# Kernel tuning notes

Hardware: AMD Instinct MI355X
Metric: run time of the kernel (lower is better)

Reference implementation:

```python
import jax, jax.numpy as jnp
import numpy as np

DIM = 768
HEADS = 12
HIDDEN = 3072  # dim * mlp_ratio
EPS = 1e-5


def layernorm(x, g, b):
    mu = jnp.mean(x, axis=-1, keepdims=True)
    var = jnp.var(x, axis=-1, keepdims=True)
    return (x - mu) * jax.lax.rsqrt(var + EPS) * g + b


def setup_inputs() -> dict:
    key = jax.random.key(0)
    ks = jax.random.split(key, 10)
    s = 0.02
    return {
        "x": jax.random.normal(ks[0], (4, 1024, DIM), jnp.float32),
        "attention_mask": jax.random.randint(ks[1], (4, 1024), 0, 2, jnp.int32),
        "ln1_g": jnp.ones((DIM,), jnp.float32),
        "ln1_b": jnp.zeros((DIM,), jnp.float32),
        "ln2_g": jnp.ones((DIM,), jnp.float32),
        "ln2_b": jnp.zeros((DIM,), jnp.float32),
        "w_qkv": jax.random.normal(ks[2], (DIM, 3 * DIM), jnp.float32) * s,
        "b_qkv": jnp.zeros((3 * DIM,), jnp.float32),
        "w_proj": jax.random.normal(ks[3], (DIM, DIM), jnp.float32) * s,
        "b_proj": jnp.zeros((DIM,), jnp.float32),
        "w_fc1": jax.random.normal(ks[4], (DIM, HIDDEN), jnp.float32) * s,
        "b_fc1": jnp.zeros((HIDDEN,), jnp.float32),
        "w_fc2": jax.random.normal(ks[5], (HIDDEN, DIM), jnp.float32) * s,
        "b_fc2": jnp.zeros((DIM,), jnp.float32),
    }


def reference(x, attention_mask, ln1_g, ln1_b, ln2_g, ln2_b,
              w_qkv, b_qkv, w_proj, b_proj, w_fc1, b_fc1, w_fc2, b_fc2):
    B, N, C = x.shape
    hd = C // HEADS
    scale = hd ** -0.5

    # --- attention branch ---
    h = layernorm(x, ln1_g, ln1_b)
    qkv = (h @ w_qkv + b_qkv).reshape(B, N, 3, HEADS, hd)
    q, k, v = qkv[:, :, 0], qkv[:, :, 1], qkv[:, :, 2]  # [B,N,H,hd]
    attn = jnp.einsum('bnhd,bmhd->bhnm', q, k) * scale
    mask_bias = jnp.where(attention_mask == 0, -10000.0, 0.0)[:, None, None, :]
    attn = jax.nn.softmax(attn + mask_bias, axis=-1)
    o = jnp.einsum('bhnm,bmhd->bnhd', attn, v).reshape(B, N, C)
    x = x + (o @ w_proj + b_proj)

    # --- MLP branch ---
    h = layernorm(x, ln2_g, ln2_b)
    h = jax.nn.gelu(h @ w_fc1 + b_fc1, approximate=False)
    x = x + (h @ w_fc2 + b_fc2)
    return x
```

## Files before the change

### kernel.cpp

```cpp
#include <hip/hip_runtime.h>

#define DIM 768
#define NTOK 4096
#define HID 3072

typedef __attribute__((ext_vector_type(8))) short bf16x8;
typedef __attribute__((ext_vector_type(4))) float f32x4;

__device__ inline unsigned short f2bf(float f){
  unsigned u = __float_as_uint(f);
  u += 0x7fff + ((u >> 16) & 1);
  return (unsigned short)(u >> 16);
}
__device__ inline unsigned cvt_pk_bf16(float a, float b){
  unsigned r;
  asm("v_cvt_pk_bf16_f32 %0, %1, %2" : "=v"(r) : "v"(a), "v"(b));
  return r;
}
__device__ inline void gload_lds16(const void* g, void* l){
  __builtin_amdgcn_global_load_lds(
      (const __attribute__((address_space(1))) unsigned int*)g,
      (__attribute__((address_space(3))) unsigned int*)l, 16, 0, 0);
}
template<int N> __device__ inline void wait_vmcnt(){
  if constexpr (N == 0) asm volatile("s_waitcnt vmcnt(0)" ::: "memory");
  else if constexpr (N == 4) asm volatile("s_waitcnt vmcnt(4)" ::: "memory");
  else if constexpr (N == 8) asm volatile("s_waitcnt vmcnt(8)" ::: "memory");
  else static_assert(N == 0, "unsupported vmcnt");
}

__global__ __launch_bounds__(256) void ln_kernel(const float* __restrict__ x,
    const float* __restrict__ g, const float* __restrict__ b,
    unsigned short* __restrict__ out)
{
  int row = blockIdx.x * 4 + (threadIdx.x >> 6);
  int lane = threadIdx.x & 63;
  const float* xr = x + (size_t)row * DIM;
  float4 v[3];
  float s = 0.f, s2 = 0.f;
#pragma unroll
  for (int j = 0; j < 3; ++j){
    v[j] = *(const float4*)(xr + j * 256 + lane * 4);
    s  += v[j].x + v[j].y + v[j].z + v[j].w;
    s2 += v[j].x*v[j].x + v[j].y*v[j].y + v[j].z*v[j].z + v[j].w*v[j].w;
  }
#pragma unroll
  for (int m = 1; m < 64; m <<= 1){ s += __shfl_xor(s, m, 64); s2 += __shfl_xor(s2, m, 64); }
  float mu  = s * (1.f / 768.f);
  float var = s2 * (1.f / 768.f) - mu * mu;
  float inv = rsqrtf(var + 1e-5f);
#pragma unroll
  for (int j = 0; j < 3; ++j){
    int c0 = j * 256 + lane * 4;
    float vv[4] = { v[j].x, v[j].y, v[j].z, v[j].w };
    ushort4 o4;
    o4.x = f2bf((vv[0] - mu) * inv * g[c0 + 0] + b[c0 + 0]);
    o4.y = f2bf((vv[1] - mu) * inv * g[c0 + 1] + b[c0 + 1]);
    o4.z = f2bf((vv[2] - mu) * inv * g[c0 + 2] + b[c0 + 2]);
    o4.w = f2bf((vv[3] - mu) * inv * g[c0 + 3] + b[c0 + 3]);
    *(ushort4*)(out + (size_t)row * DIM + c0) = o4;
  }
}

__global__ __launch_bounds__(256) void transpose4_kernel(
    const float* __restrict__ w_qkv, const float* __restrict__ w_proj,
    const float* __restrict__ w_fc1, const float* __restrict__ w_fc2,
    unsigned short* __restrict__ tq, unsigned short* __restrict__ tp,
    unsigned short* __restrict__ t1, unsigned short* __restrict__ t2)
{
  __shared__ __align__(16) unsigned short tile[32][33];
  int id = blockIdx.x;
  const float* W; unsigned short* Wt; int K, N, tx_n;
  if (id < 1728)      { W = w_qkv;  Wt = tq; K = 768;  N = 2304; tx_n = 72; }
  else if (id < 2304) { W = w_proj; Wt = tp; K = 768;  N = 768;  tx_n = 24; id -= 1728; }
  else if (id < 4608) { W = w_fc1;  Wt = t1; K = 768;  N = 3072; tx_n = 96; id -= 2304; }
  else                { W = w_fc2;  Wt = t2; K = 3072; N = 768;  tx_n = 24; id -= 4608; }
  int n0 = (id % tx_n) * 32, k0 = (id / tx_n) * 32;
  int tx = threadIdx.x & 31, ty = threadIdx.x >> 5;
#pragma unroll
  for (int i = 0; i < 32; i += 8)
    tile[ty + i][tx] = f2bf(W[(size_t)(k0 + ty + i) * N + n0 + tx]);
  __syncthreads();
#pragma unroll
  for (int i = 0; i < 32; i += 8)
    Wt[(size_t)(n0 + ty + i) * K + k0 + tx] = tile[tx][ty + i];
}

__global__ __launch_bounds__(256) void pack_mask_kernel(const int* __restrict__ am,
    unsigned long long* __restrict__ pm)
{
  int lane = threadIdx.x & 63, w = threadIdx.x >> 6, b = blockIdx.x;
  for (int k = w; k < 16; k += 4){
    unsigned long long m = __ballot(am[b * 1024 + k * 64 + lane] != 0);
    if (lane == 0) pm[b * 16 + k] = m;
  }
}

template<int DEPTH, int EPI, typename OutT>
__global__ __launch_bounds__(256) void gemm_kernel(
    const unsigned short* __restrict__ A,
    const unsigned short* __restrict__ Bt,
    const float* __restrict__ bias,
    const float* __restrict__ resid,
    OutT* __restrict__ C,
    unsigned short* __restrict__ q_out,
    unsigned short* __restrict__ k_out,
    unsigned short* __restrict__ v_out,
    int M, int N, int K)
{
  constexpr int BM = 128, BN = 128, BK = 32, WM = 64, WN = 64;
  constexpr int WAVES_N = BN / WN;
  constexpr int MI = WM / 16, NI = WN / 16;
  constexpr int ACH = BM * BK / 8, BCH = BN * BK / 8;
  constexpr int NC = (ACH + BCH) / 256;
  constexpr int SMEM_B = DEPTH * (BM + BN) * BK * 2;
  __shared__ __align__(16) char smem[SMEM_B];
  auto As = (unsigned short(*)[BM * BK])smem;
  auto Bs = (unsigned short(*)[BN * BK])(smem + DEPTH * BM * BK * 2);
  const int t = threadIdx.x, lane = t & 63, wid = t >> 6;
  const int lo = lane & 15, hi = lane >> 4;
  const int wr = wid / WAVES_N, wc = wid % WAVES_N;

  const int gx = gridDim.x;
  const int nwg = gx * gridDim.y;
  const int lin = blockIdx.y * gx + blockIdx.x;
  const int swz = (lin & 7) * (nwg >> 3) + (lin >> 3);
  const int bm = (swz / gx) * BM, bn = (swz % gx) * BN;

  auto stage = [&](int buf, int k0){
#pragma unroll
    for (int u = 0; u < NC; ++u){
      int c = u * 256 + t;
      if (c < ACH){
        gload_lds16(A + (size_t)(bm + (c >> 2)) * K + k0 + (c & 3) * 8, &As[buf][c * 8]);
      } else {
        int c2 = c - ACH;
        gload_lds16(Bt + (size_t)(bn + (c2 >> 2)) * K + k0 + (c2 & 3) * 8, &Bs[buf][c2 * 8]);
      }
    }
  };

  f32x4 acc[MI][NI];
#pragma unroll
  for (int i = 0; i < MI; ++i)
#pragma unroll
    for (int j = 0; j < NI; ++j) acc[i][j] = (f32x4){0.f, 0.f, 0.f, 0.f};

  const int NIT = K / BK;
#pragma unroll
  for (int d = 0; d < DEPTH - 1; ++d) stage(d, d * BK);
  for (int it = 0; it < NIT; ++it){
    int rem = NIT - 1 - it;
    if (rem >= DEPTH - 2) wait_vmcnt<(DEPTH - 2) * NC>();
    else if (DEPTH == 4 && rem == 1) wait_vmcnt<NC>();
    else wait_vmcnt<0>();
    __builtin_amdgcn_sched_barrier(0);
    __builtin_amdgcn_s_barrier();
    __builtin_amdgcn_sched_barrier(0);
    if (it + DEPTH - 1 < NIT) stage((it + DEPTH - 1) % DEPTH, (it + DEPTH - 1) * BK);
    const unsigned short* as = As[it % DEPTH];
    const unsigned short* bs = Bs[it % DEPTH];
    bf16x8 af[MI], bfr[NI];
#pragma unroll
    for (int i = 0; i < MI; ++i)  af[i]  = *(const bf16x8*)&as[(wr * WM + i * 16 + lo) * BK + hi * 8];
#pragma unroll
    for (int j = 0; j < NI; ++j) bfr[j] = *(const bf16x8*)&bs[(wc * WN + j * 16 + lo) * BK + hi * 8];
#pragma unroll
    for (int i = 0; i < MI; ++i)
#pragma unroll
      for (int j = 0; j < NI; ++j)
        acc[i][j] = __builtin_amdgcn_mfma_f32_16x16x32_bf16(af[i], bfr[j], acc[i][j], 0, 0, 0);
  }

  __syncthreads();

  if constexpr (EPI == 2){
    constexpr int LDE = BN + 4;
    float* ET = (float*)smem;
#pragma unroll
    for (int half = 0; half < 2; ++half){
      if (wr == half){
#pragma unroll
        for (int i = 0; i < MI; ++i)
#pragma unroll
          for (int j = 0; j < NI; ++j){
            float bcol = bias[bn + wc * WN + j * 16 + lo];
#pragma unroll
            for (int r = 0; r < 4; ++r)
              ET[(i * 16 + hi * 4 + r) * LDE + wc * WN + j * 16 + lo] = acc[i][j][r] + bcol;
          }
      }
      __syncthreads();
      int lrow = t >> 2, gg = t & 3;
      const float* rrow = resid + (size_t)(bm + half * 64 + lrow) * N + bn;
      float* crow = (float*)C + (size_t)(bm + half * 64 + lrow) * N + bn;
#pragma unroll
      for (int k = 0; k < 8; ++k){
        int c4 = (gg + k * 4) * 4;
        float4 v = *(const float4*)&ET[lrow * LDE + c4];
        float4 rs = *(const float4*)&rrow[c4];
        v.x += rs.x; v.y += rs.y; v.z += rs.z; v.w += rs.w;
        *(float4*)&crow[c4] = v;
      }
      if (half == 0) __syncthreads();
    }
  } else if constexpr (EPI == 0 || EPI == 1){
    constexpr int LDE = BN + 8;
    unsigned short* ET = (unsigned short*)smem;
#pragma unroll
    for (int i = 0; i < MI; ++i)
#pragma unroll
      for (int j = 0; j < NI; ++j){
        float bcol = bias[bn + wc * WN + j * 16 + lo];
#pragma unroll
        for (int r = 0; r < 4; ++r){
          float v = acc[i][j][r] + bcol;
          if constexpr (EPI == 1) v = 0.5f * v * (1.f + erff(v * 0.70710678118f));
          ET[(wr * WM + i * 16 + hi * 4 + r) * LDE + wc * WN + j * 16 + lo] = f2bf(v);
        }
      }
    __syncthreads();
#pragma unroll
    for (int p = 0; p < BM / 16; ++p){
      int row = p * 16 + (t >> 4), chunk = t & 15;
      *(bf16x8*)&((unsigned short*)C)[(size_t)(bm + row) * N + bn + chunk * 8] =
          *(const bf16x8*)&ET[row * LDE + chunk * 8];
    }
  } else {
    constexpr int LDE = BN + 8;
    unsigned short* ET = (unsigned short*)smem;
    const int part = bn / 768;
    const int cloc = bn % 768;
#pragma unroll
    for (int i = 0; i < MI; ++i)
#pragma unroll
      for (int j = 0; j < NI; ++j){
        int col_l = wc * WN + j * 16 + lo;
        float bcol = bias[bn + col_l];
#pragma unroll
        for (int r = 0; r < 4; ++r){
          int row_l = wr * WM + i * 16 + hi * 4 + r;
          unsigned short us = f2bf(acc[i][j][r] + bcol);
          if (part < 2) ET[row_l * LDE + col_l] = us;
          else          ET[col_l * LDE + row_l] = us;
        }
      }
    __syncthreads();
    const int bb = bm >> 10, n0b = bm & 1023;
    if (part < 2){
      unsigned short* dst0 = (part == 0) ? q_out : k_out;
#pragma unroll
      for (int p = 0; p < 8; ++p){
        int row = p * 16 + (t >> 4), chunk = t & 15;
        int hh = cloc / 64 + (chunk >> 3), d0 = (chunk & 7) * 8;
        unsigned short* dst = dst0 + ((size_t)(bb * 12 + hh)) * 65536 + (n0b + row) * 64 + d0;
        *(bf16x8*)dst = *(const bf16x8*)&ET[row * LDE + chunk * 8];
      }
    } else {
#pragma unroll
      for (int p = 0; p < 8; ++p){
        int colg = p * 16 + (t >> 4), chunk = t & 15;
        int hh = cloc / 64 + (colg >> 6), d = colg & 63;
        unsigned short* dst = v_out + ((size_t)(bb * 12 + hh)) * 65536 + (size_t)d * 1024 + n0b + chunk * 8;
        *(bf16x8*)dst = *(const bf16x8*)&ET[colg * LDE + chunk * 8];
      }
    }
  }
}

__global__ __launch_bounds__(256) void attn_kernel(
    const unsigned short* __restrict__ Qs,
    const unsigned short* __restrict__ Ks,
    const unsigned short* __restrict__ Vts,
    const unsigned long long* __restrict__ pm,
    unsigned short* __restrict__ o)
{
  constexpr int LD = 72;
  __shared__ __align__(16) unsigned short Kl[64 * LD];
  __shared__ __align__(16) unsigned short Vt[64 * LD];
  __shared__ __align__(16) unsigned short Pl[4][16 * LD];
  const int qb = blockIdx.x, h = blockIdx.y, b = blockIdx.z;
  const int t = threadIdx.x, wid = t >> 6, lane = t & 63;
  const int lo = lane & 15, hi = lane >> 4;
  const size_t bh = (size_t)b * 12 + h;

  const unsigned short* Qg = Qs + (bh * 1024 + qb * 64 + wid * 16 + lo) * 64;
  bf16x8 qf0 = *(const bf16x8*)(Qg + hi * 8);
  bf16x8 qf1 = *(const bf16x8*)(Qg + 32 + hi * 8);

  f32x4 oacc[4];
#pragma unroll
  for (int dj = 0; dj < 4; ++dj) oacc[dj] = (f32x4){0.f, 0.f, 0.f, 0.f};
  float l_part = 0.f;

  const int srow = t >> 2, scol = (t & 3) * 16;
  const unsigned short* Kg = Ks  + bh * 65536;
  const unsigned short* Vg = Vts + bh * 65536;
  unsigned short* pw = &Pl[wid][0];

  for (int kt = 0; kt < 16; ++kt){
    __syncthreads();
    const unsigned short* kg = Kg + (kt * 64 + srow) * 64 + scol;
    *(bf16x8*)&Kl[srow * LD + scol]     = *(const bf16x8*)kg;
    *(bf16x8*)&Kl[srow * LD + scol + 8] = *(const bf16x8*)(kg + 8);
    const unsigned short* vg = Vg + srow * 1024 + kt * 64 + scol;
    *(bf16x8*)&Vt[srow * LD + scol]     = *(const bf16x8*)vg;
    *(bf16x8*)&Vt[srow * LD + scol + 8] = *(const bf16x8*)(vg + 8);
    __syncthreads();

    f32x4 s[4];
#pragma unroll
    for (int nj = 0; nj < 4; ++nj) s[nj] = (f32x4){0.f, 0.f, 0.f, 0.f};
#pragma unroll
    for (int kk = 0; kk < 2; ++kk){
      bf16x8 q = kk ? qf1 : qf0;
#pragma unroll
      for (int nj = 0; nj < 4; ++nj){
        bf16x8 kf = *(const bf16x8*)&Kl[(nj * 16 + lo) * LD + kk * 32 + hi * 8];
        s[nj] = __builtin_amdgcn_mfma_f32_16x16x32_bf16(kf, q, s[nj], 0, 0, 0);
      }
    }

    unsigned long long w = pm[b * 16 + kt] >> (hi * 4);
#pragma unroll
    for (int nj = 0; nj < 4; ++nj){
      float p[4];
#pragma unroll
      for (int r = 0; r < 4; ++r){
        float e = __expf(fmaf(s[nj][r], 0.125f, -16.0f));
        e = ((unsigned)(w >> (nj * 16 + r)) & 1u) ? e : 0.0f;
        l_part += e;
        p[r] = e;
      }
      unsigned w0 = cvt_pk_bf16(p[0], p[1]);
      unsigned w1 = cvt_pk_bf16(p[2], p[3]);
      *(uint2*)&pw[lo * LD + nj * 16 + hi * 4] = make_uint2(w0, w1);
    }
    asm volatile("" ::: "memory");
    bf16x8 pf0 = *(const bf16x8*)&pw[lo * LD + hi * 8];
    bf16x8 pf1 = *(const bf16x8*)&pw[lo * LD + 32 + hi * 8];
#pragma unroll
    for (int kk = 0; kk < 2; ++kk){
      bf16x8 pf = kk ? pf1 : pf0;
#pragma unroll
      for (int dj = 0; dj < 4; ++dj){
        bf16x8 vf = *(const bf16x8*)&Vt[(dj * 16 + lo) * LD + kk * 32 + hi * 8];
        oacc[dj] = __builtin_amdgcn_mfma_f32_16x16x32_bf16(vf, pf, oacc[dj], 0, 0, 0);
      }
    }
  }

  float l = l_part;
  l += __shfl_xor(l, 16, 64);
  l += __shfl_xor(l, 32, 64);
  float inv = 1.0f / l;
  size_t orow = (size_t)b * 1024 + qb * 64 + wid * 16 + lo;
#pragma unroll
  for (int dj = 0; dj < 4; ++dj){
    unsigned w0 = (unsigned)f2bf(oacc[dj][0] * inv) | ((unsigned)f2bf(oacc[dj][1] * inv) << 16);
    unsigned w1 = (unsigned)f2bf(oacc[dj][2] * inv) | ((unsigned)f2bf(oacc[dj][3] * inv) << 16);
    *(uint2*)&o[orow * DIM + h * 64 + dj * 16 + hi * 4] = make_uint2(w0, w1);
  }
}

extern "C" void kernel_launch(void* const* d_in, const int* in_sizes, int n_in,
                              void* d_out, int out_size, void* d_ws, size_t ws_size,
                              hipStream_t stream)
{
  const float* x      = (const float*)d_in[0];
  const int*   amask  = (const int*)  d_in[1];
  const float* ln1_g  = (const float*)d_in[2];
  const float* ln1_b  = (const float*)d_in[3];
  const float* ln2_g  = (const float*)d_in[4];
  const float* ln2_b  = (const float*)d_in[5];
  const float* w_qkv  = (const float*)d_in[6];
  const float* b_qkv  = (const float*)d_in[7];
  const float* w_proj = (const float*)d_in[8];
  const float* b_proj = (const float*)d_in[9];
  const float* w_fc1  = (const float*)d_in[10];
  const float* b_fc1  = (const float*)d_in[11];
  const float* w_fc2  = (const float*)d_in[12];
  const float* b_fc2  = (const float*)d_in[13];
  float* outp = (float*)d_out;

  char* w = (char*)d_ws;
  auto alloc = [&](size_t bytes){ char* p = w; w += (bytes + 255) & ~(size_t)255; return p; };

  char* p0 = alloc((size_t)4 * 6291456);
  unsigned short* Qs   = (unsigned short*)p0;
  unsigned short* Ks   = (unsigned short*)(p0 + 6291456);
  unsigned short* Vts  = (unsigned short*)(p0 + 2 * 6291456);
  unsigned short* o_bf = (unsigned short*)(p0 + 3 * 6291456);
  unsigned short* a1   = (unsigned short*)p0;
  unsigned short* h_bf = (unsigned short*)alloc((size_t)NTOK * DIM * 2);
  unsigned short* h2   = h_bf;
  float*          x1   = (float*)alloc((size_t)NTOK * DIM * 4);
  unsigned short* wqkvT = (unsigned short*)alloc((size_t)3 * DIM * DIM * 2);
  unsigned short* wprojT= (unsigned short*)alloc((size_t)DIM * DIM * 2);
  unsigned short* wfc1T = (unsigned short*)alloc((size_t)HID * DIM * 2);
  unsigned short* wfc2T = (unsigned short*)alloc((size_t)DIM * HID * 2);
  unsigned long long* pmask = (unsigned long long*)alloc(4 * 16 * 8);

  transpose4_kernel<<<6912, 256, 0, stream>>>(w_qkv, w_proj, w_fc1, w_fc2,
                                              wqkvT, wprojT, wfc1T, wfc2T);
  pack_mask_kernel<<<4, 256, 0, stream>>>(amask, pmask);

  ln_kernel<<<NTOK / 4, 256, 0, stream>>>(x, ln1_g, ln1_b, h_bf);
  gemm_kernel<3, 3, unsigned short><<<dim3(2304 / 128, NTOK / 128), 256, 0, stream>>>(
      h_bf, wqkvT, b_qkv, nullptr, (unsigned short*)nullptr, Qs, Ks, Vts, NTOK, 2304, DIM);
  attn_kernel<<<dim3(16, 12, 4), 256, 0, stream>>>(Qs, Ks, Vts, pmask, o_bf);
  gemm_kernel<4, 2, float><<<dim3(DIM / 128, NTOK / 128), 256, 0, stream>>>(
      o_bf, wprojT, b_proj, x, x1, nullptr, nullptr, nullptr, NTOK, DIM, DIM);
  ln_kernel<<<NTOK / 4, 256, 0, stream>>>(x1, ln2_g, ln2_b, h2);
  gemm_kernel<3, 1, unsigned short><<<dim3(HID / 128, NTOK / 128), 256, 0, stream>>>(
      h2, wfc1T, b_fc1, nullptr, a1, nullptr, nullptr, nullptr, NTOK, HID, DIM);
  gemm_kernel<4, 2, float><<<dim3(DIM / 128, NTOK / 128), 256, 0, stream>>>(
      a1, wfc2T, b_fc2, x1, outp, nullptr, nullptr, nullptr, NTOK, DIM, HID);
}
```

Baseline: 183.5 us.

## Add 512-thread 128x96 GEMM kernel for N=768 residual projections

Adds a dedicated GEMM kernel with 8 waves, a 128x96 tile and BK=32 for the two N=768 GEMMs that add a residual (attention projection and fc2), replacing the generic 128x128 256-thread kernel. The smaller N tile raises the block count from 192 to 256, which fills more of the GPU's compute units on this narrow output. It also uses a deeper multi-stage global-to-LDS pipeline (4 or 6 stages) with matching vmcnt waits and an XCD-style block swizzle. The cost is fewer MFMAs per wave per K step and more barriers, which lowers arithmetic intensity per block.

After: 177.6 us. 1.03x faster.

```diff
diff --git a/kernel.cpp b/kernel.cpp
--- a/kernel.cpp
+++ b/kernel.cpp
@@ -24,7 +24,9 @@
 }
 template<int N> __device__ inline void wait_vmcnt(){
   if constexpr (N == 0) asm volatile("s_waitcnt vmcnt(0)" ::: "memory");
+  else if constexpr (N == 2) asm volatile("s_waitcnt vmcnt(2)" ::: "memory");
   else if constexpr (N == 4) asm volatile("s_waitcnt vmcnt(4)" ::: "memory");
+  else if constexpr (N == 6) asm volatile("s_waitcnt vmcnt(6)" ::: "memory");
   else if constexpr (N == 8) asm volatile("s_waitcnt vmcnt(8)" ::: "memory");
   else static_assert(N == 0, "unsupported vmcnt");
 }
@@ -174,37 +176,7 @@
 
   __syncthreads();
 
-  if constexpr (EPI == 2){
-    constexpr int LDE = BN + 4;
-    float* ET = (float*)smem;
-#pragma unroll
-    for (int half = 0; half < 2; ++half){
-      if (wr == half){
-#pragma unroll
-        for (int i = 0; i < MI; ++i)
-#pragma unroll
-          for (int j = 0; j < NI; ++j){
-            float bcol = bias[bn + wc * WN + j * 16 + lo];
-#pragma unroll
-            for (int r = 0; r < 4; ++r)
-              ET[(i * 16 + hi * 4 + r) * LDE + wc * WN + j * 16 + lo] = acc[i][j][r] + bcol;
-          }
-      }
-      __syncthreads();
-      int lrow = t >> 2, gg = t & 3;
-      const float* rrow = resid + (size_t)(bm + half * 64 + lrow) * N + bn;
-      float* crow = (float*)C + (size_t)(bm + half * 64 + lrow) * N + bn;
-#pragma unroll
-      for (int k = 0; k < 8; ++k){
-        int c4 = (gg + k * 4) * 4;
-        float4 v = *(const float4*)&ET[lrow * LDE + c4];
-        float4 rs = *(const float4*)&rrow[c4];
-        v.x += rs.x; v.y += rs.y; v.z += rs.z; v.w += rs.w;
-        *(float4*)&crow[c4] = v;
-      }
-      if (half == 0) __syncthreads();
-    }
-  } else if constexpr (EPI == 0 || EPI == 1){
+  if constexpr (EPI == 0 || EPI == 1){
     constexpr int LDE = BN + 8;
     unsigned short* ET = (unsigned short*)smem;
 #pragma unroll
@@ -264,6 +236,112 @@
         unsigned short* dst = v_out + ((size_t)(bb * 12 + hh)) * 65536 + (size_t)d * 1024 + n0b + chunk * 8;
         *(bf16x8*)dst = *(const bf16x8*)&ET[colg * LDE + chunk * 8];
       }
+    }
+  }
+}
+
+template<int DEPTH>
+__global__ __launch_bounds__(512) void gemm512_kernel(
+    const unsigned short* __restrict__ A,
+    const unsigned short* __restrict__ Bt,
+    const float* __restrict__ bias,
+    const float* __restrict__ resid,
+    float* __restrict__ C,
+    int M, int N, int K)
+{
+  constexpr int BM = 128, BN = 96, BK = 32;
+  constexpr int MI = 2, NI = 3;
+  constexpr int ACH = BM * BK / 8;
+  constexpr int BCH = BN * BK / 8;
+  constexpr int NC = 2;
+  constexpr int SMEM_B = DEPTH * (BM + BN) * BK * 2;
+  __shared__ __align__(16) char smem[SMEM_B];
+  auto As = (unsigned short(*)[BM * BK])smem;
+  auto Bs = (unsigned short(*)[BN * BK])(smem + DEPTH * BM * BK * 2);
+  const int t = threadIdx.x, lane = t & 63, wid = t >> 6;
+  const int lo = lane & 15, hi = lane >> 4;
+  const int wr = wid >> 1, wc = wid & 1;
+
+  const int gx = gridDim.x;
+  const int nwg = gx * gridDim.y;
+  const int lin = blockIdx.y * gx + blockIdx.x;
+  const int swz = (lin & 7) * (nwg >> 3) + (lin >> 3);
+  const int bm = (swz / gx) * BM, bn = (swz % gx) * BN;
+
+  auto stage = [&](int buf, int k0){
+#pragma unroll
+    for (int u = 0; u < NC; ++u){
+      int c = u * 512 + t;
+      if (c < ACH){
+        gload_lds16(A + (size_t)(bm + (c >> 2)) * K + k0 + (c & 3) * 8, &As[buf][c * 8]);
+      } else {
+        int c2 = c - ACH;
+        if (c2 >= BCH) c2 -= BCH;
+        gload_lds16(Bt + (size_t)(bn + (c2 >> 2)) * K + k0 + (c2 & 3) * 8, &Bs[buf][c2 * 8]);
+      }
+    }
+  };
+
+  f32x4 acc[MI][NI];
+#pragma unroll
+  for (int i = 0; i < MI; ++i)
+#pragma unroll
+    for (int j = 0; j < NI; ++j) acc[i][j] = (f32x4){0.f, 0.f, 0.f, 0.f};
+
+  const int NIT = K / BK;
+#pragma unroll
+  for (int d = 0; d < DEPTH - 1; ++d) stage(d, d * BK);
+  for (int it = 0; it < NIT; ++it){
+    int rem = NIT - 1 - it;
+    if (rem >= DEPTH - 2) wait_vmcnt<(DEPTH - 2) * NC>();
+    else if (rem == 3)    wait_vmcnt<6>();
+    else if (rem == 2)    wait_vmcnt<4>();
+    else if (rem == 1)    wait_vmcnt<2>();
+    else                  wait_vmcnt<0>();
+    __builtin_amdgcn_sched_barrier(0);
+    __builtin_amdgcn_s_barrier();
+    __builtin_amdgcn_sched_barrier(0);
+    if (it + DEPTH - 1 < NIT) stage((it + DEPTH - 1) % DEPTH, (it + DEPTH - 1) * BK);
+    const unsigned short* as = As[it % DEPTH];
+    const unsigned short* bs = Bs[it % DEPTH];
+    bf16x8 af[MI], bfr[NI];
+#pragma unroll
+    for (int i = 0; i < MI; ++i)  af[i]  = *(const bf16x8*)&as[(wr * 32 + i * 16 + lo) * BK + hi * 8];
+#pragma unroll
+    for (int j = 0; j < NI; ++j) bfr[j] = *(const bf16x8*)&bs[(wc * 48 + j * 16 + lo) * BK + hi * 8];
+#pragma unroll
+    for (int i = 0; i < MI; ++i)
+#pragma unroll
+      for (int j = 0; j < NI; ++j)
+        acc[i][j] = __builtin_amdgcn_mfma_f32_16x16x32_bf16(af[i], bfr[j], acc[i][j], 0, 0, 0);
+  }
+
+  __syncthreads();
+  constexpr int LDE = BN + 4;
+  static_assert(BM * LDE * 4 <= SMEM_B, "epilogue tile must fit");
+  float* ET = (float*)smem;
+#pragma unroll
+  for (int i = 0; i < MI; ++i)
+#pragma unroll
+    for (int j = 0; j < NI; ++j){
+      int col_l = wc * 48 + j * 16 + lo;
+      float bcol = bias[bn + col_l];
+#pragma unroll
+      for (int r = 0; r < 4; ++r)
+        ET[(wr * 32 + i * 16 + hi * 4 + r) * LDE + col_l] = acc[i][j][r] + bcol;
+    }
+  __syncthreads();
+  {
+    int row = t >> 2, q = t & 3;
+    const float* rrow = resid + (size_t)(bm + row) * N + bn;
+    float* crow = C + (size_t)(bm + row) * N + bn;
+#pragma unroll
+    for (int k = 0; k < 6; ++k){
+      int c4 = (q + k * 4) * 4;
+      float4 v = *(const float4*)&ET[row * LDE + c4];
+      float4 rs = *(const float4*)&rrow[c4];
+      v.x += rs.x; v.y += rs.y; v.z += rs.z; v.w += rs.w;
+      *(float4*)&crow[c4] = v;
     }
   }
 }
@@ -409,11 +487,11 @@
   gemm_kernel<3, 3, unsigned short><<<dim3(2304 / 128, NTOK / 128), 256, 0, stream>>>(
       h_bf, wqkvT, b_qkv, nullptr, (unsigned short*)nullptr, Qs, Ks, Vts, NTOK, 2304, DIM);
   attn_kernel<<<dim3(16, 12, 4), 256, 0, stream>>>(Qs, Ks, Vts, pmask, o_bf);
-  gemm_kernel<4, 2, float><<<dim3(DIM / 128, NTOK / 128), 256, 0, stream>>>(
-      o_bf, wprojT, b_proj, x, x1, nullptr, nullptr, nullptr, NTOK, DIM, DIM);
+  gemm512_kernel<4><<<dim3(DIM / 96, NTOK / 128), 512, 0, stream>>>(
+      o_bf, wprojT, b_proj, x, x1, NTOK, DIM, DIM);
   ln_kernel<<<NTOK / 4, 256, 0, stream>>>(x1, ln2_g, ln2_b, h2);
   gemm_kernel<3, 1, unsigned short><<<dim3(HID / 128, NTOK / 128), 256, 0, stream>>>(
       h2, wfc1T, b_fc1, nullptr, a1, nullptr, nullptr, nullptr, NTOK, HID, DIM);
-  gemm_kernel<4, 2, float><<<dim3(DIM / 128, NTOK / 128), 256, 0, stream>>>(
-      a1, wfc2T, b_fc2, x1, outp, nullptr, nullptr, nullptr, NTOK, DIM, HID);
-}
+  gemm512_kernel<6><<<dim3(DIM / 96, NTOK / 128), 512, 0, stream>>>(
+      a1, wfc2T, b_fc2, x1, outp, NTOK, DIM, HID);
+}
```
